# Optimization experiments

Measured on AMD Instinct MI355X. Metric: run time of the kernel, lower is better.

The kernel has to match this reference:

```python
import jax, jax.numpy as jnp
import numpy as np

N_NODES = 50000
N_EDGES = 800000
D_IN = 64
D_OUT = 64

def setup_inputs() -> dict:
    key = jax.random.key(0)
    k1, k2, k3, k4 = jax.random.split(key, 4)
    x = jax.random.normal(k1, (N_NODES, D_IN), dtype=jnp.float32)
    # Linear(in, out, bias=False): weight shape [out, in], Kaiming-uniform-ish scale
    bound = 1.0 / np.sqrt(D_IN)
    W = jax.random.uniform(k2, (D_OUT, D_IN), dtype=jnp.float32, minval=-bound, maxval=bound)
    src = jax.random.randint(k3, (N_EDGES,), 0, N_NODES, dtype=jnp.int32)
    dst = jax.random.randint(k4, (N_EDGES,), 0, N_NODES, dtype=jnp.int32)
    return {"x": x, "W": W, "src": src, "dst": dst}

def reference(x, W, src, dst):
    # update_all(copy_src, sum): for each edge (s, d), add x[s] into node d
    agg = jax.ops.segment_sum(x[src], dst, num_segments=N_NODES)  # [N, D_IN]
    # linear1 (bias=False); dropout is identity at inference
    h = jnp.einsum('nd,od->no', agg, W)  # [N, D_OUT]
    h = jax.nn.relu(h)
    # is_normalize=False -> skip L2 normalize; residual adds input node features
    return h + x
```

## Files before the change

### kernel.cpp

```cpp
#include <hip/hip_runtime.h>

#define D 64
#define NCHUNK 256
#define CAP 48

__device__ __forceinline__ float bflo(unsigned u) { return __uint_as_float(u << 16); }
__device__ __forceinline__ float bfhi(unsigned u) { return __uint_as_float(u & 0xffff0000u); }
__device__ __forceinline__ unsigned short f2bf(float f) {
    unsigned b = __float_as_uint(f);
    return (unsigned short)((b + 0x7fffu + ((b >> 16) & 1u)) >> 16);
}

__device__ __forceinline__ void gemm_body(
    int grp, int tid, float4* lds4, const float* __restrict__ x,
    const float* __restrict__ W, unsigned short* __restrict__ ybf, int n_nodes) {
    float4* As4 = lds4;
    float4* Wc4 = lds4 + 2048;
    const float4* W4 = (const float4*)W;
    for (int i = tid; i < 1024; i += 512) {
        const int kc = i >> 6, o = i & 63;
        Wc4[i] = W4[o * 16 + kc];
    }
    const int base = grp * 128;
    const float4* x4 = (const float4*)x;
#pragma unroll
    for (int r = 0; r < 4; ++r) {
        const int i = r * 512 + tid;
        const int row = i >> 4, col = i & 15;
        const int gidx = base * 16 + i;
        if (gidx < n_nodes * 16) As4[row * 16 + (col ^ (row & 15))] = x4[gidx];
    }
    __syncthreads();
    const int q = tid & 15, g = tid >> 4;
    float acc[4][4];
#pragma unroll
    for (int j = 0; j < 4; ++j)
#pragma unroll
        for (int i = 0; i < 4; ++i) acc[j][i] = 0.f;
    for (int kc = 0; kc < 16; ++kc) {
        float4 a[4], wv[4];
#pragma unroll
        for (int j = 0; j < 4; ++j) {
            const int rr = g * 4 + j;
            a[j] = As4[rr * 16 + (kc ^ (rr & 15))];
        }
#pragma unroll
        for (int i = 0; i < 4; ++i) wv[i] = Wc4[kc * 64 + q + 16 * i];
#pragma unroll
        for (int j = 0; j < 4; ++j)
#pragma unroll
            for (int i = 0; i < 4; ++i) {
                acc[j][i] = fmaf(a[j].x, wv[i].x, acc[j][i]);
                acc[j][i] = fmaf(a[j].y, wv[i].y, acc[j][i]);
                acc[j][i] = fmaf(a[j].z, wv[i].z, acc[j][i]);
                acc[j][i] = fmaf(a[j].w, wv[i].w, acc[j][i]);
            }
    }
#pragma unroll
    for (int j = 0; j < 4; ++j) {
        const int n = base + g * 4 + j;
        if (n >= n_nodes) break;
#pragma unroll
        for (int i = 0; i < 4; ++i)
            ybf[(size_t)n * D + q + 16 * i] = f2bf(acc[j][i]);
    }
}

__global__ __launch_bounds__(512) void hist_gemm_kernel(
    const int* __restrict__ dst, unsigned int* __restrict__ bh32,
    const float* __restrict__ x, const float* __restrict__ W,
    unsigned short* __restrict__ ybf, int n_nodes, int ne) {
    __shared__ float4 lds4[3136];
    const int tid = threadIdx.x;
    if ((int)blockIdx.x < NCHUNK) {
        unsigned int* lds = (unsigned int*)lds4;
        const int nw = (n_nodes + 3) >> 2;
        const int c = blockIdx.x;
        const int csz = (ne + NCHUNK - 1) / NCHUNK;
        const int e0 = c * csz, e1 = min(e0 + csz, ne);
        for (int i = tid; i < nw; i += 512) lds[i] = 0;
        __syncthreads();
        for (int e = e0 + tid; e < e1; e += 512) {
            const int d = dst[e];
            atomicAdd(&lds[d >> 2], 1u << ((d & 3) * 8));
        }
        __syncthreads();
        unsigned int* bh = bh32 + (size_t)c * nw;
        for (int i = tid; i < nw; i += 512) bh[i] = lds[i];
        return;
    }
    gemm_body((int)blockIdx.x - NCHUNK, tid, lds4, x, W, ybf, n_nodes);
}

__global__ __launch_bounds__(512) void colscan_gemm_kernel(
    const float* __restrict__ x, const float* __restrict__ W,
    unsigned char* __restrict__ bh8, int* __restrict__ counts,
    unsigned short* __restrict__ ybf, int n_nodes, int ne, int csb, int grpoff) {
    __shared__ float4 lds4[3136];
    const int tid = threadIdx.x;
    if ((int)blockIdx.x < csb) {
        const int d = blockIdx.x * 512 + tid;
        if (d >= n_nodes) return;
        const size_t npad4 = (size_t)((n_nodes + 3) >> 2) * 4;
        int acc = 0;
        for (int c0 = 0; c0 < NCHUNK; c0 += 8) {
            unsigned char v[8];
#pragma unroll
            for (int k = 0; k < 8; ++k) v[k] = bh8[(size_t)(c0 + k) * npad4 + d];
#pragma unroll
            for (int k = 0; k < 8; ++k) {
                bh8[(size_t)(c0 + k) * npad4 + d] = (unsigned char)acc;
                acc += v[k];
            }
        }
        counts[d] = acc;
        return;
    }
    gemm_body(grpoff + (int)blockIdx.x - csb, tid, lds4, x, W, ybf, n_nodes);
}

__global__ __launch_bounds__(512) void place_kernel(
    const int* __restrict__ src, const int* __restrict__ dst,
    const unsigned int* __restrict__ bh32, int* __restrict__ esrc,
    int n_nodes, int ne) {
    __shared__ unsigned int lw[12544];
    const int c = blockIdx.x;
    const int csz = (ne + NCHUNK - 1) / NCHUNK;
    const int e0 = c * csz, e1 = min(e0 + csz, ne);
    const int nw = (n_nodes + 3) >> 2;
    const unsigned int* bh = bh32 + (size_t)c * nw;
    for (int i = threadIdx.x; i < nw; i += 512) lw[i] = bh[i];
    __syncthreads();
    for (int e = e0 + threadIdx.x; e < e1; e += 512) {
        const int d = dst[e];
        const unsigned old = atomicAdd(&lw[d >> 2], 1u << ((d & 3) * 8));
        const int slot = (old >> ((d & 3) * 8)) & 0xff;
        if (slot < CAP) esrc[d * CAP + slot] = src[e];
    }
}

__global__ void gather_kernel(const int* __restrict__ counts, const int* __restrict__ esrc,
                              const unsigned short* __restrict__ ybf,
                              const float* __restrict__ x, float* __restrict__ out,
                              int n_nodes) {
    const int tid = threadIdx.x;
    const int w = tid >> 6, lane = tid & 63;
    const int g = lane >> 3, m = lane & 7;
    const uint4* Y4 = (const uint4*)ybf;
    const float4* x4 = (const float4*)x;
    float4* out4 = (float4*)out;
    const int nWaves = gridDim.x * 4;

    int n = blockIdx.x * 4 + w;
    int c = 0, s_all = 0;
    if (n < n_nodes) {
        c = min(counts[n], CAP);
        s_all = (lane < c) ? esrc[n * CAP + lane] : 0;
    }
    while (n < n_nodes) {
        const int n2 = n + nWaves;
        int c2 = 0, s2 = 0;
        if (n2 < n_nodes) {
            c2 = min(counts[n2], CAP);
            s2 = (lane < c2) ? esrc[n2 * CAP + lane] : 0;
        }
        float acc[8] = {0.f, 0.f, 0.f, 0.f, 0.f, 0.f, 0.f, 0.f};
        for (int j = 0; j < c; j += 8) {
            const int e = j + g;
            const int s = __shfl(s_all, e);
            if (e < c) {
                const uint4 v = Y4[(size_t)s * 8 + m];
                acc[0] += bflo(v.x); acc[1] += bfhi(v.x);
                acc[2] += bflo(v.y); acc[3] += bfhi(v.y);
                acc[4] += bflo(v.z); acc[5] += bfhi(v.z);
                acc[6] += bflo(v.w); acc[7] += bfhi(v.w);
            }
        }
#pragma unroll
        for (int k = 0; k < 8; ++k) {
            acc[k] += __shfl_xor(acc[k], 8);
            acc[k] += __shfl_xor(acc[k], 16);
            acc[k] += __shfl_xor(acc[k], 32);
        }
        if (lane < 8) {
            const float4 xa = x4[(size_t)n * 16 + lane * 2];
            const float4 xb = x4[(size_t)n * 16 + lane * 2 + 1];
            float4 oa, ob;
            oa.x = fmaxf(acc[0], 0.f) + xa.x;
            oa.y = fmaxf(acc[1], 0.f) + xa.y;
            oa.z = fmaxf(acc[2], 0.f) + xa.z;
            oa.w = fmaxf(acc[3], 0.f) + xa.w;
            ob.x = fmaxf(acc[4], 0.f) + xb.x;
            ob.y = fmaxf(acc[5], 0.f) + xb.y;
            ob.z = fmaxf(acc[6], 0.f) + xb.z;
            ob.w = fmaxf(acc[7], 0.f) + xb.w;
            out4[(size_t)n * 16 + lane * 2] = oa;
            out4[(size_t)n * 16 + lane * 2 + 1] = ob;
        }
        n = n2; c = c2; s_all = s2;
    }
}

extern "C" void kernel_launch(void* const* d_in, const int* in_sizes, int n_in,
                              void* d_out, int out_size, void* d_ws, size_t ws_size,
                              hipStream_t stream) {
    const float* x = (const float*)d_in[0];
    const float* W = (const float*)d_in[1];
    const int* src = (const int*)d_in[2];
    const int* dst = (const int*)d_in[3];
    float* out = (float*)d_out;

    const int n_nodes = in_sizes[0] / D;
    const int n_edges = in_sizes[2];
    const int nw = (n_nodes + 3) >> 2;

    unsigned int* bh32 = (unsigned int*)d_ws;
    int* counts = (int*)(bh32 + (size_t)NCHUNK * nw);
    int* esrc = counts + n_nodes;
    unsigned short* ybf = (unsigned short*)(esrc + (size_t)n_nodes * CAP);

    const int ngrp = (n_nodes + 127) / 128;
    const int g1 = (ngrp + 1) / 2;
    const int g2 = ngrp - g1;
    const int csb = (n_nodes + 511) / 512;

    hist_gemm_kernel<<<NCHUNK + g1, 512, 0, stream>>>(
        dst, bh32, x, W, ybf, n_nodes, n_edges);
    colscan_gemm_kernel<<<csb + g2, 512, 0, stream>>>(
        x, W, (unsigned char*)bh32, counts, ybf, n_nodes, n_edges, csb, g1);
    place_kernel<<<NCHUNK, 512, 0, stream>>>(src, dst, bh32, esrc, n_nodes, n_edges);
    gather_kernel<<<2048, 256, 0, stream>>>(counts, esrc, ybf, x, out, n_nodes);
}
```

Baseline: 132.2 us.

## Replace per-wave gather with block-level edge-balanced aggregation via LDS atomics

The gather step used to give one wave to each node and loop over that node's edge count, which leaves lanes idle when degrees differ. It is replaced by a kernel that builds a compacted edge list for 32 nodes per block in LDS. The block then spreads those edges evenly across all threads and accumulates the bf16 rows with LDS float atomics before applying ReLU and the residual. The column-scan unroll also grows from 8 to 16. The new scheme costs three extra syncs, a serial prefix sum on one thread and many LDS atomics, in exchange for better load balance. It also changes the floating-point summation order.

```diff
diff --git a/kernel.cpp b/kernel.cpp
--- a/kernel.cpp
+++ b/kernel.cpp
@@ -3,6 +3,7 @@
 #define D 64
 #define NCHUNK 256
 #define CAP 48
+#define TN 32
 
 __device__ __forceinline__ float bflo(unsigned u) { return __uint_as_float(u << 16); }
 __device__ __forceinline__ float bfhi(unsigned u) { return __uint_as_float(u & 0xffff0000u); }
@@ -103,12 +104,12 @@
         if (d >= n_nodes) return;
         const size_t npad4 = (size_t)((n_nodes + 3) >> 2) * 4;
         int acc = 0;
-        for (int c0 = 0; c0 < NCHUNK; c0 += 8) {
-            unsigned char v[8];
-#pragma unroll
-            for (int k = 0; k < 8; ++k) v[k] = bh8[(size_t)(c0 + k) * npad4 + d];
-#pragma unroll
-            for (int k = 0; k < 8; ++k) {
+        for (int c0 = 0; c0 < NCHUNK; c0 += 16) {
+            unsigned char v[16];
+#pragma unroll
+            for (int k = 0; k < 16; ++k) v[k] = bh8[(size_t)(c0 + k) * npad4 + d];
+#pragma unroll
+            for (int k = 0; k < 16; ++k) {
                 bh8[(size_t)(c0 + k) * npad4 + d] = (unsigned char)acc;
                 acc += v[k];
             }
@@ -139,65 +140,73 @@
     }
 }
 
-__global__ void gather_kernel(const int* __restrict__ counts, const int* __restrict__ esrc,
-                              const unsigned short* __restrict__ ybf,
-                              const float* __restrict__ x, float* __restrict__ out,
-                              int n_nodes) {
+__global__ __launch_bounds__(256) void agg_kernel(
+    const int* __restrict__ counts, const int* __restrict__ esrc,
+    const unsigned short* __restrict__ ybf,
+    const float* __restrict__ x, float* __restrict__ out, int n_nodes) {
+    __shared__ float accs[TN * 65];
+    __shared__ unsigned wl[TN * CAP];
+    __shared__ int cnt[TN];
+    __shared__ int wbase[TN + 1];
     const int tid = threadIdx.x;
-    const int w = tid >> 6, lane = tid & 63;
-    const int g = lane >> 3, m = lane & 7;
+    const int nb = blockIdx.x * TN;
+
+    if (tid < TN) {
+        const int ng = nb + tid;
+        cnt[tid] = (ng < n_nodes) ? min(counts[ng], CAP) : 0;
+    }
+    float4* a4 = (float4*)accs;
+    for (int i = tid; i < TN * 65 / 4; i += 256) a4[i] = make_float4(0.f, 0.f, 0.f, 0.f);
+    __syncthreads();
+    if (tid == 0) {
+        int t = 0;
+#pragma unroll
+        for (int i = 0; i < TN; ++i) { wbase[i] = t; t += cnt[i]; }
+        wbase[TN] = t;
+    }
+    __syncthreads();
+    for (int i = tid; i < TN * 64; i += 256) {
+        const int n = i >> 6, s = i & 63;
+        if (s < cnt[n])
+            wl[wbase[n] + s] = ((unsigned)n << 16) | (unsigned)esrc[(nb + n) * CAP + s];
+    }
+    __syncthreads();
+
+    const int E = wbase[TN];
+    const int m = tid & 7;
     const uint4* Y4 = (const uint4*)ybf;
-    const float4* x4 = (const float4*)x;
-    float4* out4 = (float4*)out;
-    const int nWaves = gridDim.x * 4;
-
-    int n = blockIdx.x * 4 + w;
-    int c = 0, s_all = 0;
-    if (n < n_nodes) {
-        c = min(counts[n], CAP);
-        s_all = (lane < c) ? esrc[n * CAP + lane] : 0;
-    }
-    while (n < n_nodes) {
-        const int n2 = n + nWaves;
-        int c2 = 0, s2 = 0;
-        if (n2 < n_nodes) {
-            c2 = min(counts[n2], CAP);
-            s2 = (lane < c2) ? esrc[n2 * CAP + lane] : 0;
-        }
-        float acc[8] = {0.f, 0.f, 0.f, 0.f, 0.f, 0.f, 0.f, 0.f};
-        for (int j = 0; j < c; j += 8) {
-            const int e = j + g;
-            const int s = __shfl(s_all, e);
-            if (e < c) {
-                const uint4 v = Y4[(size_t)s * 8 + m];
-                acc[0] += bflo(v.x); acc[1] += bfhi(v.x);
-                acc[2] += bflo(v.y); acc[3] += bfhi(v.y);
-                acc[4] += bflo(v.z); acc[5] += bfhi(v.z);
-                acc[6] += bflo(v.w); acc[7] += bfhi(v.w);
-            }
-        }
-#pragma unroll
-        for (int k = 0; k < 8; ++k) {
-            acc[k] += __shfl_xor(acc[k], 8);
-            acc[k] += __shfl_xor(acc[k], 16);
-            acc[k] += __shfl_xor(acc[k], 32);
-        }
-        if (lane < 8) {
-            const float4 xa = x4[(size_t)n * 16 + lane * 2];
-            const float4 xb = x4[(size_t)n * 16 + lane * 2 + 1];
-            float4 oa, ob;
-            oa.x = fmaxf(acc[0], 0.f) + xa.x;
-            oa.y = fmaxf(acc[1], 0.f) + xa.y;
-            oa.z = fmaxf(acc[2], 0.f) + xa.z;
-            oa.w = fmaxf(acc[3], 0.f) + xa.w;
-            ob.x = fmaxf(acc[4], 0.f) + xb.x;
-            ob.y = fmaxf(acc[5], 0.f) + xb.y;
-            ob.z = fmaxf(acc[6], 0.f) + xb.z;
-            ob.w = fmaxf(acc[7], 0.f) + xb.w;
-            out4[(size_t)n * 16 + lane * 2] = oa;
-            out4[(size_t)n * 16 + lane * 2 + 1] = ob;
-        }
-        n = n2; c = c2; s_all = s2;
+    for (int e = (tid >> 3); e < E; e += 32) {
+        const unsigned u = wl[e];
+        const int dl = (int)(u >> 16);
+        const int s = (int)(u & 0xffffu);
+        const uint4 v = Y4[(size_t)s * 8 + m];
+        float* a = &accs[dl * 65 + m * 8];
+        atomicAdd(&a[0], bflo(v.x)); atomicAdd(&a[1], bfhi(v.x));
+        atomicAdd(&a[2], bflo(v.y)); atomicAdd(&a[3], bfhi(v.y));
+        atomicAdd(&a[4], bflo(v.z)); atomicAdd(&a[5], bfhi(v.z));
+        atomicAdd(&a[6], bflo(v.w)); atomicAdd(&a[7], bfhi(v.w));
+    }
+    __syncthreads();
+
+    const int n = tid >> 3;
+    const int ng = nb + n;
+    if (ng < n_nodes) {
+        const float4* x4 = (const float4*)x;
+        float4* out4 = (float4*)out;
+        const float* a = &accs[n * 65 + m * 8];
+        const float4 xa = x4[(size_t)ng * 16 + m * 2];
+        const float4 xb = x4[(size_t)ng * 16 + m * 2 + 1];
+        float4 oa, ob;
+        oa.x = fmaxf(a[0], 0.f) + xa.x;
+        oa.y = fmaxf(a[1], 0.f) + xa.y;
+        oa.z = fmaxf(a[2], 0.f) + xa.z;
+        oa.w = fmaxf(a[3], 0.f) + xa.w;
+        ob.x = fmaxf(a[4], 0.f) + xb.x;
+        ob.y = fmaxf(a[5], 0.f) + xb.y;
+        ob.z = fmaxf(a[6], 0.f) + xb.z;
+        ob.w = fmaxf(a[7], 0.f) + xb.w;
+        out4[(size_t)ng * 16 + m * 2] = oa;
+        out4[(size_t)ng * 16 + m * 2 + 1] = ob;
     }
 }
 
@@ -223,11 +232,12 @@
     const int g1 = (ngrp + 1) / 2;
     const int g2 = ngrp - g1;
     const int csb = (n_nodes + 511) / 512;
+    const int nagg = (n_nodes + TN - 1) / TN;
 
     hist_gemm_kernel<<<NCHUNK + g1, 512, 0, stream>>>(
         dst, bh32, x, W, ybf, n_nodes, n_edges);
     colscan_gemm_kernel<<<csb + g2, 512, 0, stream>>>(
         x, W, (unsigned char*)bh32, counts, ybf, n_nodes, n_edges, csb, g1);
     place_kernel<<<NCHUNK, 512, 0, stream>>>(src, dst, bh32, esrc, n_nodes, n_edges);
-    gather_kernel<<<2048, 256, 0, stream>>>(counts, esrc, ybf, x, out, n_nodes);
-}
+    agg_kernel<<<nagg, 256, 0, stream>>>(counts, esrc, ybf, x, out, n_nodes);
+}
```

Result: slower. 410.7 us (+210.6%).
